# Kernel optimization log

Measured on AMD Instinct MI355X. Metric: run time of the kernel, lower is better.

## Reference

```python
import jax, jax.numpy as jnp
import numpy as np


def setup_inputs() -> dict:
    key = jax.random.key(0)
    k1, k2, k3 = jax.random.split(key, 3)
    B, C, T, H, W = 1, 3, 3, 2160, 3840
    frame_stack = jax.random.normal(k1, (B, C, T, H, W), dtype=jnp.float32)
    # learnable params: row_shifts in pixels (a few px), temporal alphas in [-1, 1]
    row_shifts = jax.random.normal(k2, (H,), dtype=jnp.float32) * 2.0
    row_temporal_shifts = jax.random.uniform(k3, (H // 2,), dtype=jnp.float32, minval=-1.0, maxval=1.0)
    return {"frame_stack": frame_stack, "row_shifts": row_shifts,
            "row_temporal_shifts": row_temporal_shifts}


def _forward(frame_stack, row_shifts, row_temporal_shifts):
    B, C, T, H, W = frame_stack.shape
    dtype = frame_stack.dtype
    # grid_sample(align_corners=False) with grid_y = pixel centers -> vertical is identity.
    # Horizontal source position in pixel coords: pos[h, j] = j - row_shifts[h]
    cols = jnp.arange(W, dtype=dtype)                      # (W,)
    pos = cols[None, :] - row_shifts[:, None]              # (H, W)
    x0 = jnp.floor(pos)
    w1 = (pos - x0).astype(dtype)                          # right-tap bilinear weight
    x0i = x0.astype(jnp.int32)
    x1i = x0i + 1
    m0 = ((x0i >= 0) & (x0i < W)).astype(dtype)            # zero padding masks
    m1 = ((x1i >= 0) & (x1i < W)).astype(dtype)
    i0 = jnp.clip(x0i, 0, W - 1)[None, None, None]         # (1,1,1,H,W)
    i1 = jnp.clip(x1i, 0, W - 1)[None, None, None]
    # gather both taps for all 3 frames at once along W
    v0 = jnp.take_along_axis(frame_stack, jnp.broadcast_to(i0, frame_stack.shape), axis=-1)
    v1 = jnp.take_along_axis(frame_stack, jnp.broadcast_to(i1, frame_stack.shape), axis=-1)
    shifted = (1.0 - w1) * m0 * v0 + w1 * m1 * v1          # (B,C,3,H,W)
    prev, cur, nxt = shifted[:, :, 0], shifted[:, :, 1], shifted[:, :, 2]
    # alpha per row: zeros on even rows, learnable on odd rows
    alpha = jnp.zeros((H,), dtype=dtype).at[1::2].set(row_temporal_shifts)
    a = alpha[None, None, :, None]                         # (1,1,H,1)
    out = jnp.where(a <= 0,
                    (1.0 + a) * cur - a * prev,
                    (1.0 - a) * cur + a * nxt)
    return out


def reference(frame_stack, row_shifts, row_temporal_shifts):
    return _forward(frame_stack, row_shifts, row_temporal_shifts)
```

## Files before the change

kernel.cpp:

```cpp
#include <hip/hip_runtime.h>

#define W_DIM 3840
#define H_DIM 2160
#define C_DIM 3
#define TPB 192
#define COLS_PER_BLOCK (TPB * 4)

__device__ __forceinline__ float4 hblend(float4 lo, float4 hi, int r,
                                         float c0, float c1) {
    float a0, a1, a2, a3, a4;
    switch (r) {
        case 0:  a0 = lo.x; a1 = lo.y; a2 = lo.z; a3 = lo.w; a4 = hi.x; break;
        case 1:  a0 = lo.y; a1 = lo.z; a2 = lo.w; a3 = hi.x; a4 = hi.y; break;
        case 2:  a0 = lo.z; a1 = lo.w; a2 = hi.x; a3 = hi.y; a4 = hi.z; break;
        default: a0 = lo.w; a1 = hi.x; a2 = hi.y; a3 = hi.z; a4 = hi.w; break;
    }
    return make_float4(c0 * a0 + c1 * a1,
                       c0 * a1 + c1 * a2,
                       c0 * a2 + c1 * a3,
                       c0 * a3 + c1 * a4);
}

__global__ __launch_bounds__(TPB) void rts_kernel(
    const float* __restrict__ fs,
    const float* __restrict__ row_shifts,
    const float* __restrict__ rts,
    float* __restrict__ out)
{
    const int h  = blockIdx.y;
    const int c  = blockIdx.z;
    const int blk_w0 = blockIdx.x * COLS_PER_BLOCK;
    const int w0 = blk_w0 + threadIdx.x * 4;

    const float shift = row_shifts[h];
    const float negs  = -shift;
    const float Kf    = floorf(negs);
    const float w1    = negs - Kf;
    const int   K     = (int)Kf;
    const float c0    = 1.0f - w1;
    const float c1    = w1;

    float a = 0.0f;
    if (h & 1) a = rts[h >> 1];
    const float ab = fabsf(a);

    const size_t frame_stride = (size_t)H_DIM * W_DIM;
    const float* curRow = fs + ((size_t)c * 3 + 1) * frame_stride + (size_t)h * W_DIM;
    const float* othRow = (a < 0.0f) ? (curRow - frame_stride)
                                     : (curRow + frame_stride);

    const bool fast = (blk_w0 + K >= 0) &&
                      (blk_w0 + COLS_PER_BLOCK + K <= W_DIM - 1);

    float4 result;
    if (fast) {
        const int base = w0 + K;
        const int A    = base & ~3;
        const int r    = base & 3;

        const float4 clo = *(const float4*)(curRow + A);
        const float4 chi = *(const float4*)(curRow + A + 4);
        result = hblend(clo, chi, r, c0, c1);

        if (ab != 0.0f) {
            const float4 olo = *(const float4*)(othRow + A);
            const float4 ohi = *(const float4*)(othRow + A + 4);
            const float4 oth = hblend(olo, ohi, r, c0, c1);
            result.x = (1.0f - ab) * result.x + ab * oth.x;
            result.y = (1.0f - ab) * result.y + ab * oth.y;
            result.z = (1.0f - ab) * result.z + ab * oth.z;
            result.w = (1.0f - ab) * result.w + ab * oth.w;
        }
    } else {
        float r4[4];
#pragma unroll
        for (int j = 0; j < 4; ++j) {
            const int x0i = w0 + j + K;
            const int x1i = x0i + 1;
            const float m0 = (x0i >= 0 && x0i < W_DIM) ? 1.0f : 0.0f;
            const float m1 = (x1i >= 0 && x1i < W_DIM) ? 1.0f : 0.0f;
            const int i0 = min(max(x0i, 0), W_DIM - 1);
            const int i1 = min(max(x1i, 0), W_DIM - 1);
            float v = c0 * m0 * curRow[i0] + c1 * m1 * curRow[i1];
            if (ab != 0.0f) {
                const float o = c0 * m0 * othRow[i0] + c1 * m1 * othRow[i1];
                v = (1.0f - ab) * v + ab * o;
            }
            r4[j] = v;
        }
        result = make_float4(r4[0], r4[1], r4[2], r4[3]);
    }

    *(float4*)(out + ((size_t)c * H_DIM + h) * W_DIM + w0) = result;
}

extern "C" void kernel_launch(void* const* d_in, const int* in_sizes, int n_in,
                              void* d_out, int out_size, void* d_ws, size_t ws_size,
                              hipStream_t stream) {
    const float* fs = (const float*)d_in[0];
    const float* rs = (const float*)d_in[1];
    const float* rt = (const float*)d_in[2];
    float* out = (float*)d_out;

    dim3 grid(W_DIM / COLS_PER_BLOCK, H_DIM, C_DIM);
    rts_kernel<<<grid, TPB, 0, stream>>>(fs, rs, rt, out);
}
```

Baseline: 53.89 us.

## Process full rows per block with nontemporal stores and per-segment edge handling

Each block now covers an entire 3840-wide row, with each thread handling five float4 segments instead of one, which cuts the block count fivefold. Per-row setup (shift, alpha, pointers) is amortized across more work, and the alpha==0 test is hoisted out of the loop into two separate unrolled paths. Output writes use nontemporal stores to avoid polluting cache. The slow path is now chosen per segment rather than per block. The trade-offs are fewer blocks (6480) and more registers per thread.

```diff
diff --git a/kernel.cpp b/kernel.cpp
--- a/kernel.cpp
+++ b/kernel.cpp
@@ -4,10 +4,12 @@
 #define H_DIM 2160
 #define C_DIM 3
 #define TPB 192
-#define COLS_PER_BLOCK (TPB * 4)
+#define NSEG 5
 
-__device__ __forceinline__ float4 hblend(float4 lo, float4 hi, int r,
-                                         float c0, float c1) {
+typedef float f32x4 __attribute__((ext_vector_type(4)));
+
+__device__ __forceinline__ f32x4 hblend(f32x4 lo, f32x4 hi, int r,
+                                        float c0, float c1) {
     float a0, a1, a2, a3, a4;
     switch (r) {
         case 0:  a0 = lo.x; a1 = lo.y; a2 = lo.z; a3 = lo.w; a4 = hi.x; break;
@@ -15,10 +17,30 @@
         case 2:  a0 = lo.z; a1 = lo.w; a2 = hi.x; a3 = hi.y; a4 = hi.z; break;
         default: a0 = lo.w; a1 = hi.x; a2 = hi.y; a3 = hi.z; a4 = hi.w; break;
     }
-    return make_float4(c0 * a0 + c1 * a1,
-                       c0 * a1 + c1 * a2,
-                       c0 * a2 + c1 * a3,
-                       c0 * a3 + c1 * a4);
+    f32x4 out;
+    out.x = c0 * a0 + c1 * a1;
+    out.y = c0 * a1 + c1 * a2;
+    out.z = c0 * a2 + c1 * a3;
+    out.w = c0 * a3 + c1 * a4;
+    return out;
+}
+
+__device__ __forceinline__ f32x4 hblend_slow(const float* __restrict__ row,
+                                             int base, float c0, float c1) {
+    f32x4 res;
+    float r4[4];
+#pragma unroll
+    for (int jj = 0; jj < 4; ++jj) {
+        const int x0i = base + jj;
+        const int x1i = x0i + 1;
+        const float m0 = (x0i >= 0 && x0i < W_DIM) ? 1.0f : 0.0f;
+        const float m1 = (x1i >= 0 && x1i < W_DIM) ? 1.0f : 0.0f;
+        const int i0 = min(max(x0i, 0), W_DIM - 1);
+        const int i1 = min(max(x1i, 0), W_DIM - 1);
+        r4[jj] = c0 * m0 * row[i0] + c1 * m1 * row[i1];
+    }
+    res.x = r4[0]; res.y = r4[1]; res.z = r4[2]; res.w = r4[3];
+    return res;
 }
 
 __global__ __launch_bounds__(TPB) void rts_kernel(
@@ -27,10 +49,9 @@
     const float* __restrict__ rts,
     float* __restrict__ out)
 {
-    const int h  = blockIdx.y;
-    const int c  = blockIdx.z;
-    const int blk_w0 = blockIdx.x * COLS_PER_BLOCK;
-    const int w0 = blk_w0 + threadIdx.x * 4;
+    const int h   = blockIdx.x;
+    const int c   = blockIdx.y;
+    const int tid = threadIdx.x;
 
     const float shift = row_shifts[h];
     const float negs  = -shift;
@@ -39,59 +60,58 @@
     const int   K     = (int)Kf;
     const float c0    = 1.0f - w1;
     const float c1    = w1;
+    const int   r     = K & 3;
 
     float a = 0.0f;
     if (h & 1) a = rts[h >> 1];
     const float ab = fabsf(a);
+    const float cw = 1.0f - ab;
 
     const size_t frame_stride = (size_t)H_DIM * W_DIM;
     const float* curRow = fs + ((size_t)c * 3 + 1) * frame_stride + (size_t)h * W_DIM;
     const float* othRow = (a < 0.0f) ? (curRow - frame_stride)
                                      : (curRow + frame_stride);
+    float* outRow = out + ((size_t)c * H_DIM + h) * W_DIM;
 
-    const bool fast = (blk_w0 + K >= 0) &&
-                      (blk_w0 + COLS_PER_BLOCK + K <= W_DIM - 1);
-
-    float4 result;
-    if (fast) {
-        const int base = w0 + K;
-        const int A    = base & ~3;
-        const int r    = base & 3;
-
-        const float4 clo = *(const float4*)(curRow + A);
-        const float4 chi = *(const float4*)(curRow + A + 4);
-        result = hblend(clo, chi, r, c0, c1);
-
-        if (ab != 0.0f) {
-            const float4 olo = *(const float4*)(othRow + A);
-            const float4 ohi = *(const float4*)(othRow + A + 4);
-            const float4 oth = hblend(olo, ohi, r, c0, c1);
-            result.x = (1.0f - ab) * result.x + ab * oth.x;
-            result.y = (1.0f - ab) * result.y + ab * oth.y;
-            result.z = (1.0f - ab) * result.z + ab * oth.z;
-            result.w = (1.0f - ab) * result.w + ab * oth.w;
+    if (ab == 0.0f) {
+#pragma unroll
+        for (int j = 0; j < NSEG; ++j) {
+            const int w0   = 4 * (tid + j * TPB);
+            const int base = w0 + K;
+            f32x4 res;
+            if (base >= 0 && base <= W_DIM - 5) {
+                const int A = base & ~3;
+                const f32x4 clo = *(const f32x4*)(curRow + A);
+                const f32x4 chi = *(const f32x4*)(curRow + A + 4);
+                res = hblend(clo, chi, r, c0, c1);
+            } else {
+                res = hblend_slow(curRow, base, c0, c1);
+            }
+            __builtin_nontemporal_store(res, (f32x4*)(outRow + w0));
         }
     } else {
-        float r4[4];
 #pragma unroll
-        for (int j = 0; j < 4; ++j) {
-            const int x0i = w0 + j + K;
-            const int x1i = x0i + 1;
-            const float m0 = (x0i >= 0 && x0i < W_DIM) ? 1.0f : 0.0f;
-            const float m1 = (x1i >= 0 && x1i < W_DIM) ? 1.0f : 0.0f;
-            const int i0 = min(max(x0i, 0), W_DIM - 1);
-            const int i1 = min(max(x1i, 0), W_DIM - 1);
-            float v = c0 * m0 * curRow[i0] + c1 * m1 * curRow[i1];
-            if (ab != 0.0f) {
-                const float o = c0 * m0 * othRow[i0] + c1 * m1 * othRow[i1];
-                v = (1.0f - ab) * v + ab * o;
+        for (int j = 0; j < NSEG; ++j) {
+            const int w0   = 4 * (tid + j * TPB);
+            const int base = w0 + K;
+            f32x4 res;
+            if (base >= 0 && base <= W_DIM - 5) {
+                const int A = base & ~3;
+                const f32x4 clo = *(const f32x4*)(curRow + A);
+                const f32x4 chi = *(const f32x4*)(curRow + A + 4);
+                const f32x4 olo = *(const f32x4*)(othRow + A);
+                const f32x4 ohi = *(const f32x4*)(othRow + A + 4);
+                const f32x4 cu  = hblend(clo, chi, r, c0, c1);
+                const f32x4 ot  = hblend(olo, ohi, r, c0, c1);
+                res = cw * cu + ab * ot;
+            } else {
+                const f32x4 cu = hblend_slow(curRow, base, c0, c1);
+                const f32x4 ot = hblend_slow(othRow, base, c0, c1);
+                res = cw * cu + ab * ot;
             }
-            r4[j] = v;
+            __builtin_nontemporal_store(res, (f32x4*)(outRow + w0));
         }
-        result = make_float4(r4[0], r4[1], r4[2], r4[3]);
     }
-
-    *(float4*)(out + ((size_t)c * H_DIM + h) * W_DIM + w0) = result;
 }
 
 extern "C" void kernel_launch(void* const* d_in, const int* in_sizes, int n_in,
@@ -102,6 +122,6 @@
     const float* rt = (const float*)d_in[2];
     float* out = (float*)d_out;
 
-    dim3 grid(W_DIM / COLS_PER_BLOCK, H_DIM, C_DIM);
+    dim3 grid(H_DIM, C_DIM);
     rts_kernel<<<grid, TPB, 0, stream>>>(fs, rs, rt, out);
 }
```

New measurement: 44.76 us. -16.9%, faster.
